# Kernel tuning notes

Measured on AMD Instinct MI355X. Metric: run time of the kernel, lower is better.

The kernel has to match this reference:

```python
import jax, jax.numpy as jnp
import numpy as np

IN_C, HID_C, OUT_C = 128, 256, 128
N_NODES, N_EDGES = 50000, 600000


def setup_inputs() -> dict:
    key = jax.random.key(0)
    ks = jax.random.split(key, 8)
    x = jax.random.normal(ks[0], (N_NODES, IN_C), dtype=jnp.float32)
    edge_index = jax.random.randint(ks[1], (2, N_EDGES), 0, N_NODES, dtype=jnp.int64)
    def glorot(k, shape):
        lim = np.sqrt(6.0 / (shape[0] + shape[1])).astype(np.float32)
        return jax.random.uniform(k, shape, dtype=jnp.float32, minval=-lim, maxval=lim)
    # PyG SAGEConv: out = lin_l(mean_aggr) + lin_r(x_root); bias only in lin_l
    W1_l = glorot(ks[2], (IN_C, HID_C)); b1 = jnp.zeros((HID_C,), jnp.float32)
    W1_r = glorot(ks[3], (IN_C, HID_C))
    W2_l = glorot(ks[4], (HID_C, OUT_C)); b2 = jnp.zeros((OUT_C,), jnp.float32)
    W2_r = glorot(ks[5], (HID_C, OUT_C))
    return {"x": x, "edge_index": edge_index, "W1_l": W1_l, "b1": b1, "W1_r": W1_r,
            "W2_l": W2_l, "b2": b2, "W2_r": W2_r}


def _sage_conv(x, src, dst, W_l, b, W_r):
    n = x.shape[0]
    msg = x[src]  # [E, C] gather from source nodes
    agg = jax.ops.segment_sum(msg, dst, num_segments=n)
    cnt = jax.ops.segment_sum(jnp.ones((src.shape[0],), x.dtype), dst, num_segments=n)
    agg = agg / jnp.maximum(cnt, 1.0)[:, None]  # mean aggregation, zero-deg safe
    return agg @ W_l + b + x @ W_r


def reference(x, edge_index, W1_l, b1, W1_r, W2_l, b2, W2_r):
    src, dst = edge_index[0], edge_index[1]
    h = jax.nn.relu(_sage_conv(x, src, dst, W1_l, b1, W1_r))
    return _sage_conv(h, src, dst, W2_l, b2, W2_r)
```

## Files before the change

### kernel.cpp

```cpp
#include <hip/hip_runtime.h>
#include <hip/hip_bf16.h>


#define N_NODES 50000
#define IN_C    128
#define HID_C   256
#define OUT_C   128
#define N_EDGES 600000
#define SLOTS   64

#define PB_FILL 586
#define PB_W1   (PB_FILL + 256)
#define PB_W2   (PB_W1 + 256)
#define PB_X    (PB_W2 + 6250)

typedef __attribute__((ext_vector_type(8))) short short8;
typedef __attribute__((ext_vector_type(4))) float f32x4;
typedef __attribute__((ext_vector_type(2))) float f32x2;

__device__ __forceinline__ float bf2f(short s) {
    union { unsigned u; float f; } c;
    c.u = ((unsigned)(unsigned short)s) << 16;
    return c.f;
}
__device__ __forceinline__ unsigned f2fp8(float v) {
    return (unsigned)__builtin_amdgcn_cvt_pk_fp8_f32(v, v, 0, false) & 0xffu;
}
__device__ __forceinline__ void acc_fp8x4(float* a, unsigned u) {
    f32x2 lo = __builtin_amdgcn_cvt_pk_f32_fp8(u, false);
    f32x2 hi = __builtin_amdgcn_cvt_pk_f32_fp8(u, true);
    a[0] += lo[0]; a[1] += lo[1]; a[2] += hi[0]; a[3] += hi[1];
}

__global__ __launch_bounds__(256) void prep(
    const float* __restrict__ x, __hip_bfloat16* __restrict__ A1,
    const float* __restrict__ W1l, const float* __restrict__ W1r,
    const float* __restrict__ W2l, const float* __restrict__ W2r,
    __hip_bfloat16* __restrict__ W1t, __hip_bfloat16* __restrict__ W2t,
    const int* __restrict__ srcI, const int* __restrict__ dstI,
    int* __restrict__ cur, int* __restrict__ colp) {
    int b = blockIdx.x;
    if (b < PB_FILL) {
        int base = b * 1024 + threadIdx.x;
        #pragma unroll
        for (int k = 0; k < 4; ++k) {
            int e = base + k * 256;
            if (e < N_EDGES) {
                int d = dstI[e];
                int pos = atomicAdd(&cur[d], 1);
                if (pos < SLOTS) colp[(size_t)d * SLOTS + pos] = srcI[e];
            }
        }
    } else if (b < PB_W1) {
        int reg = b - PB_FILL;
        int half = reg >> 7;
        int t = (reg & 127) * 256 + threadIdx.x;
        int k = t >> 8, n = t & 255;
        const float* src = half ? W1r : W1l;
        W1t[n * 256 + half * 128 + k] = __float2bfloat16(src[t]);
    } else if (b < PB_W2) {
        int reg = b - PB_W1;
        int half = reg >> 7;
        int t = (reg & 127) * 256 + threadIdx.x;
        int k = t >> 7, n = t & 127;
        const float* src = half ? W2r : W2l;
        W2t[(size_t)(half * 128 + n) * 256 + k] = __float2bfloat16(src[t]);
    } else {
        int t = (b - PB_W2) * 256 + threadIdx.x;
        if (t >= N_NODES * 32) return;
        int row = t >> 5, c = (t & 31) * 4;
        float4 v = *(const float4*)(x + (size_t)row * 128 + c);
        __hip_bfloat16* d = A1 + (size_t)row * 256 + 128 + c;
        __hip_bfloat162 p0, p1;
        p0.x = __float2bfloat16(v.x); p0.y = __float2bfloat16(v.y);
        p1.x = __float2bfloat16(v.z); p1.y = __float2bfloat16(v.w);
        *(__hip_bfloat162*)d = p0;
        *(__hip_bfloat162*)(d + 2) = p1;
    }
}

__global__ __launch_bounds__(256) void aggregate_bf16(
    const __hip_bfloat16* __restrict__ feat, int featStride,
    const int* __restrict__ deg, const int* __restrict__ colp,
    __hip_bfloat16* __restrict__ outp, int outStride, int nNodes) {
    int node = blockIdx.x * 16 + (threadIdx.x >> 4);
    int sl   = threadIdx.x & 15;
    if (node >= nNodes) return;
    int beg = node * SLOTS;
    int d   = deg[node]; if (d > SLOTS) d = SLOTS;
    const int* col = colp;
    const __hip_bfloat16* base = feat + sl * 8;
    float a[8];
    #pragma unroll
    for (int c = 0; c < 8; ++c) a[c] = 0.f;

    short8 v0, v1, v2, v3;
    int j = 0;
    if (d >= 4) {
        int s0 = col[beg + 0], s1 = col[beg + 1];
        int s2 = col[beg + 2], s3 = col[beg + 3];
        v0 = *(const short8*)(base + (size_t)s0 * featStride);
        v1 = *(const short8*)(base + (size_t)s1 * featStride);
        v2 = *(const short8*)(base + (size_t)s2 * featStride);
        v3 = *(const short8*)(base + (size_t)s3 * featStride);
        for (; j + 8 <= d; j += 4) {
            int t0 = col[beg + j + 4], t1 = col[beg + j + 5];
            int t2 = col[beg + j + 6], t3 = col[beg + j + 7];
            short8 w0 = *(const short8*)(base + (size_t)t0 * featStride);
            short8 w1 = *(const short8*)(base + (size_t)t1 * featStride);
            short8 w2 = *(const short8*)(base + (size_t)t2 * featStride);
            short8 w3 = *(const short8*)(base + (size_t)t3 * featStride);
            #pragma unroll
            for (int c = 0; c < 8; ++c)
                a[c] += (bf2f(v0[c]) + bf2f(v1[c])) + (bf2f(v2[c]) + bf2f(v3[c]));
            v0 = w0; v1 = w1; v2 = w2; v3 = w3;
        }
        #pragma unroll
        for (int c = 0; c < 8; ++c)
            a[c] += (bf2f(v0[c]) + bf2f(v1[c])) + (bf2f(v2[c]) + bf2f(v3[c]));
        j += 4;
    }
    int rem = d - j;
    if (rem > 0) {
        int s0 = col[beg + j];
        int s1 = (rem > 1) ? col[beg + j + 1] : s0;
        int s2 = (rem > 2) ? col[beg + j + 2] : s0;
        short8 t0 = *(const short8*)(base + (size_t)s0 * featStride);
        short8 t1 = *(const short8*)(base + (size_t)s1 * featStride);
        short8 t2 = *(const short8*)(base + (size_t)s2 * featStride);
        #pragma unroll
        for (int c = 0; c < 8; ++c) a[c] += bf2f(t0[c]);
        if (rem > 1) {
            #pragma unroll
            for (int c = 0; c < 8; ++c) a[c] += bf2f(t1[c]);
        }
        if (rem > 2) {
            #pragma unroll
            for (int c = 0; c < 8; ++c) a[c] += bf2f(t2[c]);
        }
    }

    float inv = 1.f / (float)max(d, 1);
    __hip_bfloat16* o = outp + (size_t)node * outStride + sl * 8;
    short8 q;
    #pragma unroll
    for (int c = 0; c < 8; ++c) {
        union { __hip_bfloat16 b; short s; } cv;
        cv.b = __float2bfloat16(a[c] * inv);
        q[c] = cv.s;
    }
    *(short8*)o = q;
}

__global__ __launch_bounds__(256) void aggregate_fp8_final(
    const unsigned char* __restrict__ feat,
    const int* __restrict__ deg, const int* __restrict__ colp,
    float* __restrict__ outp, const float* __restrict__ pre, int nNodes) {
    int node = blockIdx.x * 16 + (threadIdx.x >> 4);
    int sl   = threadIdx.x & 15;
    if (node >= nNodes) return;
    int beg = node * SLOTS;
    int d   = deg[node]; if (d > SLOTS) d = SLOTS;
    const int* col = colp;
    const unsigned char* base = feat + sl * 8;
    float a[8];
    #pragma unroll
    for (int c = 0; c < 8; ++c) a[c] = 0.f;

    uint2 v0, v1, v2, v3;
    int j = 0;
    if (d >= 4) {
        int s0 = col[beg + 0], s1 = col[beg + 1];
        int s2 = col[beg + 2], s3 = col[beg + 3];
        v0 = *(const uint2*)(base + (size_t)s0 * 128);
        v1 = *(const uint2*)(base + (size_t)s1 * 128);
        v2 = *(const uint2*)(base + (size_t)s2 * 128);
        v3 = *(const uint2*)(base + (size_t)s3 * 128);
        for (; j + 8 <= d; j += 4) {
            int t0 = col[beg + j + 4], t1 = col[beg + j + 5];
            int t2 = col[beg + j + 6], t3 = col[beg + j + 7];
            uint2 w0 = *(const uint2*)(base + (size_t)t0 * 128);
            uint2 w1 = *(const uint2*)(base + (size_t)t1 * 128);
            uint2 w2 = *(const uint2*)(base + (size_t)t2 * 128);
            uint2 w3 = *(const uint2*)(base + (size_t)t3 * 128);
            acc_fp8x4(a,     v0.x); acc_fp8x4(a,     v1.x);
            acc_fp8x4(a,     v2.x); acc_fp8x4(a,     v3.x);
            acc_fp8x4(a + 4, v0.y); acc_fp8x4(a + 4, v1.y);
            acc_fp8x4(a + 4, v2.y); acc_fp8x4(a + 4, v3.y);
            v0 = w0; v1 = w1; v2 = w2; v3 = w3;
        }
        acc_fp8x4(a,     v0.x); acc_fp8x4(a,     v1.x);
        acc_fp8x4(a,     v2.x); acc_fp8x4(a,     v3.x);
        acc_fp8x4(a + 4, v0.y); acc_fp8x4(a + 4, v1.y);
        acc_fp8x4(a + 4, v2.y); acc_fp8x4(a + 4, v3.y);
        j += 4;
    }
    for (; j < d; ++j) {
        uint2 v = *(const uint2*)(base + (size_t)col[beg + j] * 128);
        acc_fp8x4(a, v.x);
        acc_fp8x4(a + 4, v.y);
    }

    float inv = 1.f / (float)max(d, 1);
    const float* pp = pre + (size_t)node * 128 + sl * 8;
    float* op = outp + (size_t)node * 128 + sl * 8;
    float4 p0 = *(const float4*)pp;
    float4 p1 = *(const float4*)(pp + 4);
    *(float4*)op       = make_float4(a[0] * inv + p0.x, a[1] * inv + p0.y,
                                     a[2] * inv + p0.z, a[3] * inv + p0.w);
    *(float4*)(op + 4) = make_float4(a[4] * inv + p1.x, a[5] * inv + p1.y,
                                     a[6] * inv + p1.z, a[7] * inv + p1.w);
}


#define GBM 128
#define GBN 128
#define GBK 64
#define EP_STRIDE_BF 132

__device__ __forceinline__ void gload16(const void* g, void* l) {
    typedef const __attribute__((address_space(1))) unsigned int* gp_t;
    typedef __attribute__((address_space(3))) unsigned int* lp_t;
    __builtin_amdgcn_global_load_lds((gp_t)g, (lp_t)l, 16, 0, 0);
}

__global__ __launch_bounds__(256) void gemm_mfma(
    const __hip_bfloat16* __restrict__ A, int lda,
    const __hip_bfloat16* __restrict__ Bt,
    const float* __restrict__ bias,
    __hip_bfloat16* __restrict__ outBf,
    int M, int K) {
    __shared__ char sm[GBM * EP_STRIDE_BF * 2];
    __hip_bfloat16* Als = (__hip_bfloat16*)sm;
    __hip_bfloat16* Bls = (__hip_bfloat16*)(sm + GBM * GBK * 2);

    int tid  = threadIdx.x;
    int wave = tid >> 6, lane = tid & 63;
    int wm = wave >> 1, wn = wave & 1;
    int mb = blockIdx.x * GBM, nb = blockIdx.y * GBN;

    int srow_base = wave * 32;
    int lrow = lane >> 3;
    int pch  = lane & 7;

    f32x4 acc[4][4];
    #pragma unroll
    for (int i = 0; i < 4; ++i)
        #pragma unroll
        for (int j = 0; j < 4; ++j)
            acc[i][j] = (f32x4){0.f, 0.f, 0.f, 0.f};

    for (int kt = 0; kt < K; kt += GBK) {
        #pragma unroll
        for (int t = 0; t < 4; ++t) {
            int rloc = srow_base + t * 8 + lrow;
            int lch  = pch ^ (rloc & 7);
            int ga_row = mb + rloc; if (ga_row >= M) ga_row = M - 1;
            const __hip_bfloat16* ga = A + (size_t)ga_row * lda + kt + lch * 8;
            gload16(ga, &Als[(srow_base + t * 8) * GBK]);
            const __hip_bfloat16* gb = Bt + (size_t)(nb + rloc) * K + kt + lch * 8;
            gload16(gb, &Bls[(srow_base + t * 8) * GBK]);
        }
        __syncthreads();

        #pragma unroll
        for (int ks = 0; ks < GBK; ks += 32) {
            int chunkL = (ks >> 3) + (lane >> 4);
            short8 af[4], bf[4];
            #pragma unroll
            for (int i = 0; i < 4; ++i) {
                int row = wm * 64 + i * 16 + (lane & 15);
                int pc  = chunkL ^ (row & 7);
                af[i] = *(const short8*)&Als[row * GBK + pc * 8];
            }
            #pragma unroll
            for (int j = 0; j < 4; ++j) {
                int row = wn * 64 + j * 16 + (lane & 15);
                int pc  = chunkL ^ (row & 7);
                bf[j] = *(const short8*)&Bls[row * GBK + pc * 8];
            }
            #pragma unroll
            for (int i = 0; i < 4; ++i)
                #pragma unroll
                for (int j = 0; j < 4; ++j)
                    acc[i][j] = __builtin_amdgcn_mfma_f32_16x16x32_bf16(
                        af[i], bf[j], acc[i][j], 0, 0, 0);
        }
        __syncthreads();
    }

    int cn[4];
    float bc[4];
    __hip_bfloat16* sb = (__hip_bfloat16*)sm;
    #pragma unroll
    for (int j = 0; j < 4; ++j) {
        cn[j] = wn * 64 + j * 16 + (lane & 15);
        bc[j] = bias[nb + cn[j]];
    }
    #pragma unroll
    for (int i = 0; i < 4; ++i)
        #pragma unroll
        for (int r = 0; r < 4; ++r) {
            int lr = wm * 64 + i * 16 + (lane >> 4) * 4 + r;
            #pragma unroll
            for (int j = 0; j < 4; ++j)
                sb[lr * EP_STRIDE_BF + cn[j]] =
                    __float2bfloat16(fmaxf(acc[i][j][r] + bc[j], 0.f));
        }
    __syncthreads();
    #pragma unroll
    for (int it = 0; it < 8; ++it) {
        int chunk = it * 256 + tid;
        int lr  = chunk >> 4;
        int lcB = (chunk & 15) * 16;
        int grow = mb + lr;
        if (grow < M)
            *(float4*)((char*)outBf + (size_t)grow * 512 + nb * 2 + lcB) =
                *(const float4*)((const char*)sb + lr * (EP_STRIDE_BF * 2) + lcB);
    }
}

#define GBM2 64

__global__ __launch_bounds__(256) void gemm2_fused(
    const __hip_bfloat16* __restrict__ A,
    const __hip_bfloat16* __restrict__ Bt,
    const float* __restrict__ b2,
    unsigned char* __restrict__ outF8,
    float* __restrict__ outF,
    int M) {
    __shared__ __hip_bfloat16 Als[GBM2 * GBK];
    __shared__ __hip_bfloat16 Bls[256 * GBK];

    int tid  = threadIdx.x;
    int wave = tid >> 6, lane = tid & 63;
    int mb = blockIdx.x * GBM2;
    int lrow = lane >> 3;
    int pch  = lane & 7;

    f32x4 acc[4][4];
    #pragma unroll
    for (int i = 0; i < 4; ++i)
        #pragma unroll
        for (int j = 0; j < 4; ++j)
            acc[i][j] = (f32x4){0.f, 0.f, 0.f, 0.f};

    for (int kt = 0; kt < 256; kt += GBK) {
        #pragma unroll
        for (int t = 0; t < 2; ++t) {
            int g = wave * 2 + t;
            int rloc = g * 8 + lrow;
            int lch  = pch ^ (rloc & 7);
            int ga_row = mb + rloc; if (ga_row >= M) ga_row = M - 1;
            gload16(A + (size_t)ga_row * 256 + kt + lch * 8, &Als[g * 8 * GBK]);
        }
        #pragma unroll
        for (int t = 0; t < 8; ++t) {
            int g = wave * 8 + t;
            int rloc = g * 8 + lrow;
            int lch  = pch ^ (rloc & 7);
            gload16(Bt + (size_t)rloc * 256 + kt + lch * 8, &Bls[g * 8 * GBK]);
        }
        __syncthreads();

        #pragma unroll
        for (int ks = 0; ks < GBK; ks += 32) {
            int chunkL = (ks >> 3) + (lane >> 4);
            short8 af[4], bf[4];
            #pragma unroll
            for (int i = 0; i < 4; ++i) {
                int row = i * 16 + (lane & 15);
                int pc  = chunkL ^ (row & 7);
                af[i] = *(const short8*)&Als[row * GBK + pc * 8];
            }
            #pragma unroll
            for (int j = 0; j < 4; ++j) {
                int row = wave * 64 + j * 16 + (lane & 15);
                int pc  = chunkL ^ (row & 7);
                bf[j] = *(const short8*)&Bls[row * GBK + pc * 8];
            }
            #pragma unroll
            for (int i = 0; i < 4; ++i)
                #pragma unroll
                for (int j = 0; j < 4; ++j)
                    acc[i][j] = __builtin_amdgcn_mfma_f32_16x16x32_bf16(
                        af[i], bf[j], acc[i][j], 0, 0, 0);
        }
        __syncthreads();
    }

    int cn[4];
    #pragma unroll
    for (int j = 0; j < 4; ++j) cn[j] = wave * 64 + j * 16 + (lane & 15);
    if (wave < 2) {
        #pragma unroll
        for (int i = 0; i < 4; ++i)
            #pragma unroll
            for (int r = 0; r < 4; ++r) {
                int row = mb + i * 16 + (lane >> 4) * 4 + r;
                if (row >= M) continue;
                #pragma unroll
                for (int j = 0; j < 4; ++j)
                    outF8[(size_t)row * 128 + cn[j]] = (unsigned char)f2fp8(acc[i][j][r]);
            }
    } else {
        float bc[4];
        #pragma unroll
        for (int j = 0; j < 4; ++j) bc[j] = b2[cn[j] - 128];
        #pragma unroll
        for (int i = 0; i < 4; ++i)
            #pragma unroll
            for (int r = 0; r < 4; ++r) {
                int row = mb + i * 16 + (lane >> 4) * 4 + r;
                if (row >= M) continue;
                #pragma unroll
                for (int j = 0; j < 4; ++j)
                    outF[(size_t)row * 128 + cn[j] - 128] = acc[i][j][r] + bc[j];
            }
    }
}

extern "C" void kernel_launch(void* const* d_in, const int* in_sizes, int n_in,
                              void* d_out, int out_size, void* d_ws, size_t ws_size,
                              hipStream_t stream) {
    const float* x    = (const float*)d_in[0];
    const int*   ei   = (const int*)d_in[1];
    const float* W1l  = (const float*)d_in[2];
    const float* b1   = (const float*)d_in[3];
    const float* W1r  = (const float*)d_in[4];
    const float* W2l  = (const float*)d_in[5];
    const float* b2   = (const float*)d_in[6];
    const float* W2r  = (const float*)d_in[7];
    float* out = (float*)d_out;

    const int E = N_EDGES;
    const int N = N_NODES;
    const int* srcI = ei;
    const int* dstI = ei + E;

    char* w = (char*)d_ws;
    int*            cur     = (int*)(w + 0);
    int*            colp    = (int*)(w + 204800);
    __hip_bfloat16* W1t     = (__hip_bfloat16*)(w + 13004800);
    __hip_bfloat16* W2t     = (__hip_bfloat16*)(w + 13135872);
    __hip_bfloat16* A1      = (__hip_bfloat16*)(w + 13266944);
    __hip_bfloat16* h_bf    = (__hip_bfloat16*)(w + 38866944);
    unsigned char*  hp_f8   = (unsigned char*)(w + 64466944);
    float*          pre     = (float*)(w + 70866944);

    hipMemsetAsync(cur, 0, 200000, stream);
    prep<<<PB_X, 256, 0, stream>>>(x, A1, W1l, W1r, W2l, W2r, W1t, W2t,
                                   srcI, dstI, cur, colp);

    aggregate_bf16<<<(N + 15) / 16, 256, 0, stream>>>(
        A1 + 128, 256, cur, colp, A1, 256, N);
    {
        dim3 grid((N + GBM - 1) / GBM, HID_C / GBN);
        gemm_mfma<<<grid, 256, 0, stream>>>(A1, 256, W1t, b1, h_bf, N, 256);
    }

    gemm2_fused<<<(N + GBM2 - 1) / GBM2, 256, 0, stream>>>(
        h_bf, W2t, b2, hp_f8, pre, N);

    aggregate_fp8_final<<<(N + 15) / 16, 256, 0, stream>>>(
        hp_f8, cur, colp, out, pre, N);
}
```

Measured before the change: 197.6 us.

## Build CSR neighbor lists via shared-memory two-pass binning instead of global atomics

Replaces the per-edge global atomicAdd scatter into per-node slot lists with two kernels. The first bins edges by destination block of 256 nodes, using shared-memory counters and packed src/dst words. The second builds each node's slot list in LDS and writes it out with vector stores. The aim is to avoid heavily contended random global atomics and scattered 4-byte writes. The trade-offs are extra kernel launches, an intermediate buffer, writes of all 64 slots per node, and per-block bin caps that could silently drop edges in skewed inputs.

```diff
diff --git a/kernel.cpp b/kernel.cpp
--- a/kernel.cpp
+++ b/kernel.cpp
@@ -9,10 +9,15 @@
 #define N_EDGES 600000
 #define SLOTS   64
 
-#define PB_FILL 586
-#define PB_W1   (PB_FILL + 256)
-#define PB_W2   (PB_W1 + 256)
-#define PB_X    (PB_W2 + 6250)
+#define NBIN     196
+#define BSTRIDE  8192
+#define PA_BLOCKS 128
+#define PA_CHUNK  4688
+#define PA_CAP    64
+
+#define PB_W1   256
+#define PB_W2   512
+#define PB_X    6762
 
 typedef __attribute__((ext_vector_type(8))) short short8;
 typedef __attribute__((ext_vector_type(4))) float f32x4;
@@ -32,27 +37,78 @@
     a[0] += lo[0]; a[1] += lo[1]; a[2] += hi[0]; a[3] += hi[1];
 }
 
+__global__ __launch_bounds__(256) void bin_edges(
+    const int* __restrict__ srcI, const int* __restrict__ dstI,
+    int* __restrict__ gcur, unsigned* __restrict__ gbuf) {
+    __shared__ int lcnt[NBIN];
+    __shared__ int lbase[NBIN];
+    __shared__ unsigned lbuf[NBIN][PA_CAP];
+    int t = threadIdx.x;
+    for (int i = t; i < NBIN; i += 256) lcnt[i] = 0;
+    __syncthreads();
+    int e0 = blockIdx.x * PA_CHUNK;
+    int e1 = e0 + PA_CHUNK; if (e1 > N_EDGES) e1 = N_EDGES;
+    for (int e = e0 + t; e < e1; e += 256) {
+        int d = dstI[e];
+        int s = srcI[e];
+        int bin = d >> 8;
+        int pos = atomicAdd(&lcnt[bin], 1);
+        if (pos < PA_CAP)
+            lbuf[bin][pos] = ((unsigned)(d & 255) << 16) | (unsigned)s;
+    }
+    __syncthreads();
+    for (int b = t; b < NBIN; b += 256) {
+        int n = lcnt[b]; if (n > PA_CAP) n = PA_CAP;
+        lbase[b] = atomicAdd(&gcur[b], n);
+        lcnt[b] = n;
+    }
+    __syncthreads();
+    int wave = t >> 6, lane = t & 63;
+    for (int b = wave; b < NBIN; b += 4) {
+        int n = lcnt[b];
+        if (lane < n)
+            gbuf[(size_t)b * BSTRIDE + lbase[b] + lane] = lbuf[b][lane];
+    }
+}
+
+__global__ __launch_bounds__(256) void build_lists(
+    const unsigned* __restrict__ gbuf, const int* __restrict__ gcur,
+    int* __restrict__ colp, int* __restrict__ cnt) {
+    __shared__ int lcnt[256];
+    __shared__ int lcol[256][SLOTS];
+    int b = blockIdx.x, t = threadIdx.x;
+    lcnt[t] = 0;
+    __syncthreads();
+    int n = gcur[b];
+    const unsigned* src = gbuf + (size_t)b * BSTRIDE;
+    for (int i = t; i < n; i += 256) {
+        unsigned p = src[i];
+        int dl = (int)(p >> 16);
+        int s  = (int)(p & 0xFFFFu);
+        int pos = atomicAdd(&lcnt[dl], 1);
+        if (pos < SLOTS) lcol[dl][pos] = s;
+    }
+    __syncthreads();
+    int node0 = b * 256;
+    int nHere = N_NODES - node0; if (nHere > 256) nHere = 256;
+    if (t < nHere) cnt[node0 + t] = lcnt[t];
+    int tot = nHere * (SLOTS / 4);
+    for (int i = t; i < tot; i += 256) {
+        int node = i >> 4;
+        int sg   = i & 15;
+        *(int4*)&colp[(size_t)(node0 + node) * SLOTS + sg * 4] =
+            *(const int4*)&lcol[node][sg * 4];
+    }
+}
+
 __global__ __launch_bounds__(256) void prep(
     const float* __restrict__ x, __hip_bfloat16* __restrict__ A1,
     const float* __restrict__ W1l, const float* __restrict__ W1r,
     const float* __restrict__ W2l, const float* __restrict__ W2r,
-    __hip_bfloat16* __restrict__ W1t, __hip_bfloat16* __restrict__ W2t,
-    const int* __restrict__ srcI, const int* __restrict__ dstI,
-    int* __restrict__ cur, int* __restrict__ colp) {
+    __hip_bfloat16* __restrict__ W1t, __hip_bfloat16* __restrict__ W2t) {
     int b = blockIdx.x;
-    if (b < PB_FILL) {
-        int base = b * 1024 + threadIdx.x;
-        #pragma unroll
-        for (int k = 0; k < 4; ++k) {
-            int e = base + k * 256;
-            if (e < N_EDGES) {
-                int d = dstI[e];
-                int pos = atomicAdd(&cur[d], 1);
-                if (pos < SLOTS) colp[(size_t)d * SLOTS + pos] = srcI[e];
-            }
-        }
-    } else if (b < PB_W1) {
-        int reg = b - PB_FILL;
+    if (b < PB_W1) {
+        int reg = b;
         int half = reg >> 7;
         int t = (reg & 127) * 256 + threadIdx.x;
         int k = t >> 8, n = t & 255;
@@ -439,21 +495,24 @@
     const int* dstI = ei + E;
 
     char* w = (char*)d_ws;
-    int*            cur     = (int*)(w + 0);
-    int*            colp    = (int*)(w + 204800);
-    __hip_bfloat16* W1t     = (__hip_bfloat16*)(w + 13004800);
-    __hip_bfloat16* W2t     = (__hip_bfloat16*)(w + 13135872);
-    __hip_bfloat16* A1      = (__hip_bfloat16*)(w + 13266944);
-    __hip_bfloat16* h_bf    = (__hip_bfloat16*)(w + 38866944);
-    unsigned char*  hp_f8   = (unsigned char*)(w + 64466944);
-    float*          pre     = (float*)(w + 70866944);
-
-    hipMemsetAsync(cur, 0, 200000, stream);
-    prep<<<PB_X, 256, 0, stream>>>(x, A1, W1l, W1r, W2l, W2r, W1t, W2t,
-                                   srcI, dstI, cur, colp);
+    int*            gcur    = (int*)(w + 0);
+    unsigned*       gbuf    = (unsigned*)(w + 1024);
+    int*            cnt     = (int*)(w + 6423552);
+    int*            colp    = (int*)(w + 6624000);
+    __hip_bfloat16* W1t     = (__hip_bfloat16*)(w + 19424000);
+    __hip_bfloat16* W2t     = (__hip_bfloat16*)(w + 19555072);
+    __hip_bfloat16* A1      = (__hip_bfloat16*)(w + 19686400);
+    __hip_bfloat16* h_bf    = (__hip_bfloat16*)(w + 45286400);
+    unsigned char*  hp_f8   = (unsigned char*)(w + 70886400);
+    float*          pre     = (float*)(w + 77286400);
+
+    hipMemsetAsync(gcur, 0, 1024, stream);
+    bin_edges<<<PA_BLOCKS, 256, 0, stream>>>(srcI, dstI, gcur, gbuf);
+    prep<<<PB_X, 256, 0, stream>>>(x, A1, W1l, W1r, W2l, W2r, W1t, W2t);
+    build_lists<<<NBIN, 256, 0, stream>>>(gbuf, gcur, colp, cnt);
 
     aggregate_bf16<<<(N + 15) / 16, 256, 0, stream>>>(
-        A1 + 128, 256, cur, colp, A1, 256, N);
+        A1 + 128, 256, cnt, colp, A1, 256, N);
     {
         dim3 grid((N + GBM - 1) / GBM, HID_C / GBN);
         gemm_mfma<<<grid, 256, 0, stream>>>(A1, 256, W1t, b1, h_bf, N, 256);
@@ -463,5 +522,5 @@
         h_bf, W2t, b2, hp_f8, pre, N);
 
     aggregate_fp8_final<<<(N + 15) / 16, 256, 0, stream>>>(
-        hp_f8, cur, colp, out, pre, N);
-}
+        hp_f8, cnt, colp, out, pre, N);
+}
```

Result: no change. 199.5 us (+0.9%).

## Fuse layer-1 aggregation, both GEMMs and ReLU into one kernel

Applied to the files above, without the earlier changes.

Replaces the separate layer-1 aggregate, GEMM1 and GEMM2 kernels with one kernel per 64-node tile. Each tile gathers neighbor means plus its root features into LDS, runs GEMM1 with bias and ReLU, writes h back into LDS, then runs GEMM2 and emits the fp8 messages and the root term. This removes the global round trips of the A1 and h intermediates and two launches. The cost is a 64KB LDS footprint per block, which limits occupancy, and B weight tiles are reloaded for every 64-row block.

```diff
diff --git a/kernel.cpp b/kernel.cpp
--- a/kernel.cpp
+++ b/kernel.cpp
@@ -32,8 +32,14 @@
     a[0] += lo[0]; a[1] += lo[1]; a[2] += hi[0]; a[3] += hi[1];
 }
 
+__device__ __forceinline__ void gload16(const void* g, void* l) {
+    typedef const __attribute__((address_space(1))) unsigned int* gp_t;
+    typedef __attribute__((address_space(3))) unsigned int* lp_t;
+    __builtin_amdgcn_global_load_lds((gp_t)g, (lp_t)l, 16, 0, 0);
+}
+
 __global__ __launch_bounds__(256) void prep(
-    const float* __restrict__ x, __hip_bfloat16* __restrict__ A1,
+    const float* __restrict__ x, __hip_bfloat16* __restrict__ xbf,
     const float* __restrict__ W1l, const float* __restrict__ W1r,
     const float* __restrict__ W2l, const float* __restrict__ W2r,
     __hip_bfloat16* __restrict__ W1t, __hip_bfloat16* __restrict__ W2t,
@@ -70,7 +76,7 @@
         if (t >= N_NODES * 32) return;
         int row = t >> 5, c = (t & 31) * 4;
         float4 v = *(const float4*)(x + (size_t)row * 128 + c);
-        __hip_bfloat16* d = A1 + (size_t)row * 256 + 128 + c;
+        __hip_bfloat16* d = xbf + (size_t)row * 128 + c;
         __hip_bfloat162 p0, p1;
         p0.x = __float2bfloat16(v.x); p0.y = __float2bfloat16(v.y);
         p1.x = __float2bfloat16(v.z); p1.y = __float2bfloat16(v.w);
@@ -79,77 +85,227 @@
     }
 }
 
-__global__ __launch_bounds__(256) void aggregate_bf16(
-    const __hip_bfloat16* __restrict__ feat, int featStride,
+__global__ __launch_bounds__(256, 2) void fused_fwd(
+    const __hip_bfloat16* __restrict__ xbf,
     const int* __restrict__ deg, const int* __restrict__ colp,
-    __hip_bfloat16* __restrict__ outp, int outStride, int nNodes) {
-    int node = blockIdx.x * 16 + (threadIdx.x >> 4);
-    int sl   = threadIdx.x & 15;
-    if (node >= nNodes) return;
-    int beg = node * SLOTS;
-    int d   = deg[node]; if (d > SLOTS) d = SLOTS;
-    const int* col = colp;
-    const __hip_bfloat16* base = feat + sl * 8;
-    float a[8];
-    #pragma unroll
-    for (int c = 0; c < 8; ++c) a[c] = 0.f;
-
-    short8 v0, v1, v2, v3;
-    int j = 0;
-    if (d >= 4) {
-        int s0 = col[beg + 0], s1 = col[beg + 1];
-        int s2 = col[beg + 2], s3 = col[beg + 3];
-        v0 = *(const short8*)(base + (size_t)s0 * featStride);
-        v1 = *(const short8*)(base + (size_t)s1 * featStride);
-        v2 = *(const short8*)(base + (size_t)s2 * featStride);
-        v3 = *(const short8*)(base + (size_t)s3 * featStride);
-        for (; j + 8 <= d; j += 4) {
-            int t0 = col[beg + j + 4], t1 = col[beg + j + 5];
-            int t2 = col[beg + j + 6], t3 = col[beg + j + 7];
-            short8 w0 = *(const short8*)(base + (size_t)t0 * featStride);
-            short8 w1 = *(const short8*)(base + (size_t)t1 * featStride);
-            short8 w2 = *(const short8*)(base + (size_t)t2 * featStride);
-            short8 w3 = *(const short8*)(base + (size_t)t3 * featStride);
+    const __hip_bfloat16* __restrict__ W1t,
+    const float* __restrict__ b1,
+    const __hip_bfloat16* __restrict__ W2t,
+    const float* __restrict__ b2,
+    unsigned char* __restrict__ hp,
+    float* __restrict__ pre,
+    int M) {
+    __shared__ char sm[65536];
+    __hip_bfloat16* hAB = (__hip_bfloat16*)sm;
+    __hip_bfloat16* Bst = (__hip_bfloat16*)(sm + 32768);
+
+    int tid  = threadIdx.x;
+    int wave = tid >> 6, lane = tid & 63;
+    int mb   = blockIdx.x * 64;
+    int sl   = tid & 15;
+    int lrow = lane >> 3, pch = lane & 7;
+
+    for (int pass = 0; pass < 4; ++pass) {
+        int r = pass * 16 + (tid >> 4);
+        int node = mb + r; if (node >= M) node = M - 1;
+        int d = deg[node]; if (d > SLOTS) d = SLOTS;
+        const int* col = colp + (size_t)node * SLOTS;
+        const __hip_bfloat16* base = xbf + sl * 8;
+        float a[8];
+        #pragma unroll
+        for (int c = 0; c < 8; ++c) a[c] = 0.f;
+
+        short8 v0, v1, v2, v3;
+        int j = 0;
+        if (d >= 4) {
+            int s0 = col[0], s1 = col[1], s2 = col[2], s3 = col[3];
+            v0 = *(const short8*)(base + (size_t)s0 * 128);
+            v1 = *(const short8*)(base + (size_t)s1 * 128);
+            v2 = *(const short8*)(base + (size_t)s2 * 128);
+            v3 = *(const short8*)(base + (size_t)s3 * 128);
+            for (; j + 8 <= d; j += 4) {
+                int t0 = col[j + 4], t1 = col[j + 5];
+                int t2 = col[j + 6], t3 = col[j + 7];
+                short8 w0 = *(const short8*)(base + (size_t)t0 * 128);
+                short8 w1 = *(const short8*)(base + (size_t)t1 * 128);
+                short8 w2 = *(const short8*)(base + (size_t)t2 * 128);
+                short8 w3 = *(const short8*)(base + (size_t)t3 * 128);
+                #pragma unroll
+                for (int c = 0; c < 8; ++c)
+                    a[c] += (bf2f(v0[c]) + bf2f(v1[c])) + (bf2f(v2[c]) + bf2f(v3[c]));
+                v0 = w0; v1 = w1; v2 = w2; v3 = w3;
+            }
             #pragma unroll
             for (int c = 0; c < 8; ++c)
                 a[c] += (bf2f(v0[c]) + bf2f(v1[c])) + (bf2f(v2[c]) + bf2f(v3[c]));
-            v0 = w0; v1 = w1; v2 = w2; v3 = w3;
-        }
-        #pragma unroll
-        for (int c = 0; c < 8; ++c)
-            a[c] += (bf2f(v0[c]) + bf2f(v1[c])) + (bf2f(v2[c]) + bf2f(v3[c]));
-        j += 4;
-    }
-    int rem = d - j;
-    if (rem > 0) {
-        int s0 = col[beg + j];
-        int s1 = (rem > 1) ? col[beg + j + 1] : s0;
-        int s2 = (rem > 2) ? col[beg + j + 2] : s0;
-        short8 t0 = *(const short8*)(base + (size_t)s0 * featStride);
-        short8 t1 = *(const short8*)(base + (size_t)s1 * featStride);
-        short8 t2 = *(const short8*)(base + (size_t)s2 * featStride);
-        #pragma unroll
-        for (int c = 0; c < 8; ++c) a[c] += bf2f(t0[c]);
-        if (rem > 1) {
-            #pragma unroll
-            for (int c = 0; c < 8; ++c) a[c] += bf2f(t1[c]);
-        }
-        if (rem > 2) {
-            #pragma unroll
-            for (int c = 0; c < 8; ++c) a[c] += bf2f(t2[c]);
-        }
-    }
-
-    float inv = 1.f / (float)max(d, 1);
-    __hip_bfloat16* o = outp + (size_t)node * outStride + sl * 8;
-    short8 q;
+            j += 4;
+        }
+        int rem = d - j;
+        if (rem > 0) {
+            int s0 = col[j];
+            int s1 = (rem > 1) ? col[j + 1] : s0;
+            int s2 = (rem > 2) ? col[j + 2] : s0;
+            short8 t0 = *(const short8*)(base + (size_t)s0 * 128);
+            short8 t1 = *(const short8*)(base + (size_t)s1 * 128);
+            short8 t2 = *(const short8*)(base + (size_t)s2 * 128);
+            #pragma unroll
+            for (int c = 0; c < 8; ++c) a[c] += bf2f(t0[c]);
+            if (rem > 1) {
+                #pragma unroll
+                for (int c = 0; c < 8; ++c) a[c] += bf2f(t1[c]);
+            }
+            if (rem > 2) {
+                #pragma unroll
+                for (int c = 0; c < 8; ++c) a[c] += bf2f(t2[c]);
+            }
+        }
+
+        float inv = 1.f / (float)max(d, 1);
+        short8 q;
+        #pragma unroll
+        for (int c = 0; c < 8; ++c) {
+            union { __hip_bfloat16 b; short s; } cv;
+            cv.b = __float2bfloat16(a[c] * inv);
+            q[c] = cv.s;
+        }
+        int pc = (sl & 8) | ((sl & 7) ^ (r & 7));
+        *(short8*)&hAB[r * 256 + pc * 8] = q;
+        short8 sv = *(const short8*)(xbf + (size_t)node * 128 + sl * 8);
+        *(short8*)&hAB[r * 256 + (16 + pc) * 8] = sv;
+    }
+    __syncthreads();
+
+    f32x4 acc[4][4];
     #pragma unroll
-    for (int c = 0; c < 8; ++c) {
-        union { __hip_bfloat16 b; short s; } cv;
-        cv.b = __float2bfloat16(a[c] * inv);
-        q[c] = cv.s;
-    }
-    *(short8*)o = q;
+    for (int i = 0; i < 4; ++i)
+        #pragma unroll
+        for (int j = 0; j < 4; ++j)
+            acc[i][j] = (f32x4){0.f, 0.f, 0.f, 0.f};
+
+    for (int kt = 0; kt < 256; kt += 64) {
+        #pragma unroll
+        for (int t = 0; t < 8; ++t) {
+            int g = wave * 8 + t;
+            int rloc = g * 8 + lrow;
+            int lch  = pch ^ (rloc & 7);
+            gload16(W1t + (size_t)rloc * 256 + kt + lch * 8, &Bst[g * 8 * 64]);
+        }
+        __syncthreads();
+        #pragma unroll
+        for (int ks = 0; ks < 64; ks += 32) {
+            int chunkL = (ks >> 3) + (lane >> 4);
+            short8 af[4], bf[4];
+            #pragma unroll
+            for (int i = 0; i < 4; ++i) {
+                int row = i * 16 + (lane & 15);
+                af[i] = *(const short8*)&hAB[row * 256 +
+                        ((kt >> 3) + (chunkL ^ (row & 7))) * 8];
+            }
+            #pragma unroll
+            for (int j = 0; j < 4; ++j) {
+                int brow = wave * 64 + j * 16 + (lane & 15);
+                bf[j] = *(const short8*)&Bst[brow * 64 + (chunkL ^ (brow & 7)) * 8];
+            }
+            #pragma unroll
+            for (int i = 0; i < 4; ++i)
+                #pragma unroll
+                for (int j = 0; j < 4; ++j)
+                    acc[i][j] = __builtin_amdgcn_mfma_f32_16x16x32_bf16(
+                        af[i], bf[j], acc[i][j], 0, 0, 0);
+        }
+        __syncthreads();
+    }
+
+    int cn[4];
+    float bc[4];
+    #pragma unroll
+    for (int j = 0; j < 4; ++j) {
+        cn[j] = wave * 64 + j * 16 + (lane & 15);
+        bc[j] = b1[cn[j]];
+    }
+    #pragma unroll
+    for (int i = 0; i < 4; ++i)
+        #pragma unroll
+        for (int r = 0; r < 4; ++r) {
+            int row = i * 16 + (lane >> 4) * 4 + r;
+            #pragma unroll
+            for (int j = 0; j < 4; ++j) {
+                float v = fmaxf(acc[i][j][r] + bc[j], 0.f);
+                int c = cn[j] >> 3;
+                int pchk = (c & ~7) | ((c & 7) ^ (row & 7));
+                union { __hip_bfloat16 b; short s; } cv;
+                cv.b = __float2bfloat16(v);
+                *(short*)&hAB[row * 256 + pchk * 8 + (cn[j] & 7)] = cv.s;
+            }
+        }
+    __syncthreads();
+
+    #pragma unroll
+    for (int i = 0; i < 4; ++i)
+        #pragma unroll
+        for (int j = 0; j < 4; ++j)
+            acc[i][j] = (f32x4){0.f, 0.f, 0.f, 0.f};
+
+    for (int kt = 0; kt < 256; kt += 64) {
+        #pragma unroll
+        for (int t = 0; t < 8; ++t) {
+            int g = wave * 8 + t;
+            int rloc = g * 8 + lrow;
+            int lch  = pch ^ (rloc & 7);
+            gload16(W2t + (size_t)rloc * 256 + kt + lch * 8, &Bst[g * 8 * 64]);
+        }
+        __syncthreads();
+        #pragma unroll
+        for (int ks = 0; ks < 64; ks += 32) {
+            int chunkL = (ks >> 3) + (lane >> 4);
+            short8 af[4], bf[4];
+            #pragma unroll
+            for (int i = 0; i < 4; ++i) {
+                int row = i * 16 + (lane & 15);
+                af[i] = *(const short8*)&hAB[row * 256 +
+                        ((kt >> 3) + (chunkL ^ (row & 7))) * 8];
+            }
+            #pragma unroll
+            for (int j = 0; j < 4; ++j) {
+                int brow = wave * 64 + j * 16 + (lane & 15);
+                bf[j] = *(const short8*)&Bst[brow * 64 + (chunkL ^ (brow & 7)) * 8];
+            }
+            #pragma unroll
+            for (int i = 0; i < 4; ++i)
+                #pragma unroll
+                for (int j = 0; j < 4; ++j)
+                    acc[i][j] = __builtin_amdgcn_mfma_f32_16x16x32_bf16(
+                        af[i], bf[j], acc[i][j], 0, 0, 0);
+        }
+        __syncthreads();
+    }
+
+    if (wave < 2) {
+        #pragma unroll
+        for (int i = 0; i < 4; ++i)
+            #pragma unroll
+            for (int r = 0; r < 4; ++r) {
+                int row = mb + i * 16 + (lane >> 4) * 4 + r;
+                if (row >= M) continue;
+                #pragma unroll
+                for (int j = 0; j < 4; ++j)
+                    hp[(size_t)row * 128 + cn[j]] = (unsigned char)f2fp8(acc[i][j][r]);
+            }
+    } else {
+        float bc2[4];
+        #pragma unroll
+        for (int j = 0; j < 4; ++j) bc2[j] = b2[cn[j] - 128];
+        #pragma unroll
+        for (int i = 0; i < 4; ++i)
+            #pragma unroll
+            for (int r = 0; r < 4; ++r) {
+                int row = mb + i * 16 + (lane >> 4) * 4 + r;
+                if (row >= M) continue;
+                #pragma unroll
+                for (int j = 0; j < 4; ++j)
+                    pre[(size_t)row * 128 + cn[j] - 128] = acc[i][j][r] + bc2[j];
+            }
+    }
 }
 
 __global__ __launch_bounds__(256) void aggregate_fp8_final(
@@ -212,214 +368,6 @@
                                      a[6] * inv + p1.z, a[7] * inv + p1.w);
 }
 
-
-#define GBM 128
-#define GBN 128
-#define GBK 64
-#define EP_STRIDE_BF 132
-
-__device__ __forceinline__ void gload16(const void* g, void* l) {
-    typedef const __attribute__((address_space(1))) unsigned int* gp_t;
-    typedef __attribute__((address_space(3))) unsigned int* lp_t;
-    __builtin_amdgcn_global_load_lds((gp_t)g, (lp_t)l, 16, 0, 0);
-}
-
-__global__ __launch_bounds__(256) void gemm_mfma(
-    const __hip_bfloat16* __restrict__ A, int lda,
-    const __hip_bfloat16* __restrict__ Bt,
-    const float* __restrict__ bias,
-    __hip_bfloat16* __restrict__ outBf,
-    int M, int K) {
-    __shared__ char sm[GBM * EP_STRIDE_BF * 2];
-    __hip_bfloat16* Als = (__hip_bfloat16*)sm;
-    __hip_bfloat16* Bls = (__hip_bfloat16*)(sm + GBM * GBK * 2);
-
-    int tid  = threadIdx.x;
-    int wave = tid >> 6, lane = tid & 63;
-    int wm = wave >> 1, wn = wave & 1;
-    int mb = blockIdx.x * GBM, nb = blockIdx.y * GBN;
-
-    int srow_base = wave * 32;
-    int lrow = lane >> 3;
-    int pch  = lane & 7;
-
-    f32x4 acc[4][4];
-    #pragma unroll
-    for (int i = 0; i < 4; ++i)
-        #pragma unroll
-        for (int j = 0; j < 4; ++j)
-            acc[i][j] = (f32x4){0.f, 0.f, 0.f, 0.f};
-
-    for (int kt = 0; kt < K; kt += GBK) {
-        #pragma unroll
-        for (int t = 0; t < 4; ++t) {
-            int rloc = srow_base + t * 8 + lrow;
-            int lch  = pch ^ (rloc & 7);
-            int ga_row = mb + rloc; if (ga_row >= M) ga_row = M - 1;
-            const __hip_bfloat16* ga = A + (size_t)ga_row * lda + kt + lch * 8;
-            gload16(ga, &Als[(srow_base + t * 8) * GBK]);
-            const __hip_bfloat16* gb = Bt + (size_t)(nb + rloc) * K + kt + lch * 8;
-            gload16(gb, &Bls[(srow_base + t * 8) * GBK]);
-        }
-        __syncthreads();
-
-        #pragma unroll
-        for (int ks = 0; ks < GBK; ks += 32) {
-            int chunkL = (ks >> 3) + (lane >> 4);
-            short8 af[4], bf[4];
-            #pragma unroll
-            for (int i = 0; i < 4; ++i) {
-                int row = wm * 64 + i * 16 + (lane & 15);
-                int pc  = chunkL ^ (row & 7);
-                af[i] = *(const short8*)&Als[row * GBK + pc * 8];
-            }
-            #pragma unroll
-            for (int j = 0; j < 4; ++j) {
-                int row = wn * 64 + j * 16 + (lane & 15);
-                int pc  = chunkL ^ (row & 7);
-                bf[j] = *(const short8*)&Bls[row * GBK + pc * 8];
-            }
-            #pragma unroll
-            for (int i = 0; i < 4; ++i)
-                #pragma unroll
-                for (int j = 0; j < 4; ++j)
-                    acc[i][j] = __builtin_amdgcn_mfma_f32_16x16x32_bf16(
-                        af[i], bf[j], acc[i][j], 0, 0, 0);
-        }
-        __syncthreads();
-    }
-
-    int cn[4];
-    float bc[4];
-    __hip_bfloat16* sb = (__hip_bfloat16*)sm;
-    #pragma unroll
-    for (int j = 0; j < 4; ++j) {
-        cn[j] = wn * 64 + j * 16 + (lane & 15);
-        bc[j] = bias[nb + cn[j]];
-    }
-    #pragma unroll
-    for (int i = 0; i < 4; ++i)
-        #pragma unroll
-        for (int r = 0; r < 4; ++r) {
-            int lr = wm * 64 + i * 16 + (lane >> 4) * 4 + r;
-            #pragma unroll
-            for (int j = 0; j < 4; ++j)
-                sb[lr * EP_STRIDE_BF + cn[j]] =
-                    __float2bfloat16(fmaxf(acc[i][j][r] + bc[j], 0.f));
-        }
-    __syncthreads();
-    #pragma unroll
-    for (int it = 0; it < 8; ++it) {
-        int chunk = it * 256 + tid;
-        int lr  = chunk >> 4;
-        int lcB = (chunk & 15) * 16;
-        int grow = mb + lr;
-        if (grow < M)
-            *(float4*)((char*)outBf + (size_t)grow * 512 + nb * 2 + lcB) =
-                *(const float4*)((const char*)sb + lr * (EP_STRIDE_BF * 2) + lcB);
-    }
-}
-
-#define GBM2 64
-
-__global__ __launch_bounds__(256) void gemm2_fused(
-    const __hip_bfloat16* __restrict__ A,
-    const __hip_bfloat16* __restrict__ Bt,
-    const float* __restrict__ b2,
-    unsigned char* __restrict__ outF8,
-    float* __restrict__ outF,
-    int M) {
-    __shared__ __hip_bfloat16 Als[GBM2 * GBK];
-    __shared__ __hip_bfloat16 Bls[256 * GBK];
-
-    int tid  = threadIdx.x;
-    int wave = tid >> 6, lane = tid & 63;
-    int mb = blockIdx.x * GBM2;
-    int lrow = lane >> 3;
-    int pch  = lane & 7;
-
-    f32x4 acc[4][4];
-    #pragma unroll
-    for (int i = 0; i < 4; ++i)
-        #pragma unroll
-        for (int j = 0; j < 4; ++j)
-            acc[i][j] = (f32x4){0.f, 0.f, 0.f, 0.f};
-
-    for (int kt = 0; kt < 256; kt += GBK) {
-        #pragma unroll
-        for (int t = 0; t < 2; ++t) {
-            int g = wave * 2 + t;
-            int rloc = g * 8 + lrow;
-            int lch  = pch ^ (rloc & 7);
-            int ga_row = mb + rloc; if (ga_row >= M) ga_row = M - 1;
-            gload16(A + (size_t)ga_row * 256 + kt + lch * 8, &Als[g * 8 * GBK]);
-        }
-        #pragma unroll
-        for (int t = 0; t < 8; ++t) {
-            int g = wave * 8 + t;
-            int rloc = g * 8 + lrow;
-            int lch  = pch ^ (rloc & 7);
-            gload16(Bt + (size_t)rloc * 256 + kt + lch * 8, &Bls[g * 8 * GBK]);
-        }
-        __syncthreads();
-
-        #pragma unroll
-        for (int ks = 0; ks < GBK; ks += 32) {
-            int chunkL = (ks >> 3) + (lane >> 4);
-            short8 af[4], bf[4];
-            #pragma unroll
-            for (int i = 0; i < 4; ++i) {
-                int row = i * 16 + (lane & 15);
-                int pc  = chunkL ^ (row & 7);
-                af[i] = *(const short8*)&Als[row * GBK + pc * 8];
-            }
-            #pragma unroll
-            for (int j = 0; j < 4; ++j) {
-                int row = wave * 64 + j * 16 + (lane & 15);
-                int pc  = chunkL ^ (row & 7);
-                bf[j] = *(const short8*)&Bls[row * GBK + pc * 8];
-            }
-            #pragma unroll
-            for (int i = 0; i < 4; ++i)
-                #pragma unroll
-                for (int j = 0; j < 4; ++j)
-                    acc[i][j] = __builtin_amdgcn_mfma_f32_16x16x32_bf16(
-                        af[i], bf[j], acc[i][j], 0, 0, 0);
-        }
-        __syncthreads();
-    }
-
-    int cn[4];
-    #pragma unroll
-    for (int j = 0; j < 4; ++j) cn[j] = wave * 64 + j * 16 + (lane & 15);
-    if (wave < 2) {
-        #pragma unroll
-        for (int i = 0; i < 4; ++i)
-            #pragma unroll
-            for (int r = 0; r < 4; ++r) {
-                int row = mb + i * 16 + (lane >> 4) * 4 + r;
-                if (row >= M) continue;
-                #pragma unroll
-                for (int j = 0; j < 4; ++j)
-                    outF8[(size_t)row * 128 + cn[j]] = (unsigned char)f2fp8(acc[i][j][r]);
-            }
-    } else {
-        float bc[4];
-        #pragma unroll
-        for (int j = 0; j < 4; ++j) bc[j] = b2[cn[j] - 128];
-        #pragma unroll
-        for (int i = 0; i < 4; ++i)
-            #pragma unroll
-            for (int r = 0; r < 4; ++r) {
-                int row = mb + i * 16 + (lane >> 4) * 4 + r;
-                if (row >= M) continue;
-                #pragma unroll
-                for (int j = 0; j < 4; ++j)
-                    outF[(size_t)row * 128 + cn[j] - 128] = acc[i][j][r] + bc[j];
-            }
-    }
-}
-
 extern "C" void kernel_launch(void* const* d_in, const int* in_sizes, int n_in,
                               void* d_out, int out_size, void* d_ws, size_t ws_size,
                               hipStream_t stream) {
@@ -433,34 +381,25 @@
     const float* W2r  = (const float*)d_in[7];
     float* out = (float*)d_out;
 
-    const int E = N_EDGES;
     const int N = N_NODES;
     const int* srcI = ei;
-    const int* dstI = ei + E;
+    const int* dstI = ei + N_EDGES;
 
     char* w = (char*)d_ws;
     int*            cur     = (int*)(w + 0);
     int*            colp    = (int*)(w + 204800);
     __hip_bfloat16* W1t     = (__hip_bfloat16*)(w + 13004800);
     __hip_bfloat16* W2t     = (__hip_bfloat16*)(w + 13135872);
-    __hip_bfloat16* A1      = (__hip_bfloat16*)(w + 13266944);
-    __hip_bfloat16* h_bf    = (__hip_bfloat16*)(w + 38866944);
-    unsigned char*  hp_f8   = (unsigned char*)(w + 64466944);
-    float*          pre     = (float*)(w + 70866944);
+    __hip_bfloat16* xbf     = (__hip_bfloat16*)(w + 13266944);
+    unsigned char*  hp_f8   = (unsigned char*)(w + 26066944);
+    float*          pre     = (float*)(w + 32466944);
 
     hipMemsetAsync(cur, 0, 200000, stream);
-    prep<<<PB_X, 256, 0, stream>>>(x, A1, W1l, W1r, W2l, W2r, W1t, W2t,
+    prep<<<PB_X, 256, 0, stream>>>(x, xbf, W1l, W1r, W2l, W2r, W1t, W2t,
                                    srcI, dstI, cur, colp);
 
-    aggregate_bf16<<<(N + 15) / 16, 256, 0, stream>>>(
-        A1 + 128, 256, cur, colp, A1, 256, N);
-    {
-        dim3 grid((N + GBM - 1) / GBM, HID_C / GBN);
-        gemm_mfma<<<grid, 256, 0, stream>>>(A1, 256, W1t, b1, h_bf, N, 256);
-    }
-
-    gemm2_fused<<<(N + GBM2 - 1) / GBM2, 256, 0, stream>>>(
-        h_bf, W2t, b2, hp_f8, pre, N);
+    fused_fwd<<<(N + 63) / 64, 256, 0, stream>>>(
+        xbf, cur, colp, W1t, b1, W2t, b2, hp_f8, pre, N);
 
     aggregate_fp8_final<<<(N + 15) / 16, 256, 0, stream>>>(
         hp_f8, cur, colp, out, pre, N);
```

Result: no change. 197.0 us (-0.3%).
